# Kernel tuning notes

Hardware: AMD Instinct MI355X
Metric: run time of the kernel (lower is better)

The kernel has to match this reference:

```python
import jax, jax.numpy as jnp
import numpy as np

N = 10000        # nodes
E = 160000       # edges (avg degree 16)
MUL = 128        # channel multiplicity
A = 10           # node-attr (species one-hot) dim
RAD = 8          # radial bessel features
INV_SQRT3 = 0.5773502691896258  # CG coefficient for 1o x 1o -> 0e


def _mlp(x, Ws):
    # RadialMLP: linear layers with SiLU between, no activation on last
    for W in Ws[:-1]:
        x = jax.nn.silu(x @ W)
    return x @ Ws[-1]


def setup_inputs() -> dict:
    key = jax.random.key(0)
    ks = jax.random.split(key, 25)

    def g(k, shape):
        return jax.random.normal(k, shape, jnp.float32) / np.float32(np.sqrt(shape[0]))

    return {
        "node_attrs": jax.random.uniform(ks[0], (N, A), jnp.float32),
        "node_feats": jax.random.normal(ks[1], (N, 4 * MUL), jnp.float32),
        "edge_attrs": jax.random.normal(ks[2], (E, 4), jnp.float32),
        "edge_feats": jax.random.uniform(ks[3], (E, RAD), jnp.float32),
        "W_src": g(ks[5], (A, MUL)),
        "W_tgt": g(ks[6], (A, MUL)),
        "W_up0": g(ks[7], (MUL, MUL)),
        "W_up1": g(ks[8], (MUL, MUL)),
        "W_skip0": g(ks[9], (MUL, MUL)),
        "W_skip1": g(ks[10], (MUL, MUL)),
        "W_res0": g(ks[11], (MUL, 2 * MUL)),
        "W_res1": g(ks[12], (MUL, MUL)),
        "W_lin1_0": g(ks[13], (2 * MUL, 2 * MUL)),
        "W_lin1_1": g(ks[14], (2 * MUL, MUL)),
        "W_lin2_0": g(ks[15], (MUL, MUL)),
        "W_lin2_1": g(ks[16], (MUL, MUL)),
        "W_rad1": g(ks[17], (RAD + 2 * MUL, 64)),
        "W_rad2": g(ks[18], (64, 64)),
        "W_rad3": g(ks[19], (64, 64)),
        "W_rad4": g(ks[20], (64, 4 * MUL)),
        "W_den1": g(ks[21], (RAD + 2 * MUL, 64)),
        "W_den2": g(ks[22], (64, 1)),
        "alpha": jnp.ones((), jnp.float32),   # scaled by 20 inside (alpha = param * 20)
        "beta": jnp.zeros((), jnp.float32),
        "edge_index": jax.random.randint(ks[4], (E, 2), 0, N),
    }


def _forward(node_attrs, node_feats, edge_attrs, edge_feats,
             W_src, W_tgt, W_up0, W_up1, W_skip0, W_skip1, W_res0, W_res1,
             W_lin1_0, W_lin1_1, W_lin2_0, W_lin2_1,
             W_rad1, W_rad2, W_rad3, W_rad4, W_den1, W_den2,
             alpha, beta, edge_index):
    n = node_feats.shape[0]
    # split node feats into 128x0e scalars and 128x1o vectors (mul_ir layout)
    s = node_feats[:, :MUL]                           # [N, 128]
    v = node_feats[:, MUL:].reshape(n, MUL, 3)        # [N, 128, 3]

    # skip connection: Linear(node_feats_irreps -> hidden_irreps)
    sc_s = s @ W_skip0
    sc_v = jnp.einsum("nui,uv->nvi", v, W_skip1)
    sc = jnp.concatenate([sc_s, sc_v.reshape(n, -1)], axis=-1)  # [N, 512]

    # linear_up (node_feats -> edge_irreps) and linear_res (-> irreps_nonlin)
    up_s = s @ W_up0
    up_v = jnp.einsum("nui,uv->nvi", v, W_up1)
    res_s = s @ W_res0                                # [N, 256] (scalars + gates)
    res_v = jnp.einsum("nui,uv->nvi", v, W_res1)      # [N, 128, 3]

    # per-species scalar embeddings, gathered per edge
    src_emb = node_attrs @ W_src                      # [N, 128]
    tgt_emb = node_attrs @ W_tgt
    snd = edge_index[:, 0]
    rcv = edge_index[:, 1]
    aug = jnp.concatenate([edge_feats, src_emb[snd], tgt_emb[rcv]], axis=-1)  # [E, 264]

    # radial MLP -> per-edge tensor-product weights; density MLP
    tpw = _mlp(aug, [W_rad1, W_rad2, W_rad3, W_rad4])  # [E, 512]
    edge_density = jnp.tanh(_mlp(aug, [W_den1, W_den2]) ** 2)  # [E, 1]
    density = jax.ops.segment_sum(edge_density, rcv, num_segments=n)  # [N, 1]

    # equivariant tensor product (uvu, per-edge weights), lmax=1 CG paths
    xs = up_s[snd]                                    # [E, 128]
    xv = up_v[snd]                                    # [E, 128, 3]
    y0 = edge_attrs[:, :1]                            # [E, 1]
    y1 = edge_attrs[:, 1:4]                           # [E, 3]
    wA, wB, wC, wD = jnp.split(tpw, 4, axis=-1)
    mA = wA * xs * y0                                               # 0e x 0e -> 0e
    mD = wD * jnp.einsum("eui,ei->eu", xv, y1) * INV_SQRT3          # 1o x 1o -> 0e
    mB = (wB * xs)[:, :, None] * y1[:, None, :]                     # 0e x 1o -> 1o
    mC = wC[:, :, None] * xv * y0[:, :, None]                       # 1o x 0e -> 1o
    m_s = jnp.concatenate([mA, mD], axis=-1)          # [E, 256]
    m_v = jnp.concatenate([mB, mC], axis=1)           # [E, 256, 3]

    # scatter-add messages to receiver nodes
    msg_s = jax.ops.segment_sum(m_s, rcv, num_segments=n)  # [N, 256]
    msg_v = jax.ops.segment_sum(m_v, rcv, num_segments=n)  # [N, 256, 3]

    # linear_1 (irreps_mid -> irreps_nonlin), density normalization, residual
    msg_s = msg_s @ W_lin1_0                          # [N, 256]
    msg_v = jnp.einsum("nui,uv->nvi", msg_v, W_lin1_1)  # [N, 128, 3]
    denom = density * beta + alpha * 20.0             # [N, 1]
    msg_s = msg_s / denom + res_s
    msg_v = msg_v / denom[..., None] + res_v

    # equivariant gate nonlinearity: silu on scalars, sigmoid gates on vectors
    scal = jax.nn.silu(msg_s[:, :MUL])
    gate = jax.nn.sigmoid(msg_s[:, MUL:])
    vec = msg_v * gate[:, :, None]

    # linear_2 and reshape to [N, channels, (lmax+1)^2]
    out_s = scal @ W_lin2_0                           # [N, 128]
    out_v = jnp.einsum("nui,uv->nvi", vec, W_lin2_1)  # [N, 128, 3]
    message = jnp.concatenate([out_s[:, :, None], out_v], axis=-1)  # [N, 128, 4]
    return message, sc


def reference(node_attrs, node_feats, edge_attrs, edge_feats,
              W_src, W_tgt, W_up0, W_up1, W_skip0, W_skip1, W_res0, W_res1,
              W_lin1_0, W_lin1_1, W_lin2_0, W_lin2_1,
              W_rad1, W_rad2, W_rad3, W_rad4, W_den1, W_den2,
              alpha, beta, edge_index):
    return _forward(node_attrs, node_feats, edge_attrs, edge_feats,
                    W_src, W_tgt, W_up0, W_up1, W_skip0, W_skip1, W_res0, W_res1,
                    W_lin1_0, W_lin1_1, W_lin2_0, W_lin2_1,
                    W_rad1, W_rad2, W_rad3, W_rad4, W_den1, W_den2,
                    alpha, beta, edge_index)
```

## Files before the change

kernel.cpp:

```cpp
#include <hip/hip_runtime.h>
#include <math.h>

#define NN 10000
#define NE 160000
#define MUL 128
#define ADIM 10
#define RADF 8
#define HID 64
#define INV_SQRT3 0.57735026918962576f
#define NB64 157

typedef __attribute__((ext_vector_type(8))) short bf16x8;
typedef __attribute__((ext_vector_type(4))) float f32x4;

__device__ __forceinline__ float silu_f(float x){ return x / (1.0f + __expf(-x)); }
__device__ __forceinline__ float sigmoid_f(float x){ return 1.0f / (1.0f + __expf(-x)); }
__device__ __forceinline__ unsigned short f2b(float f){
  union{float f; unsigned u;} v; v.f=f;
  unsigned r = (v.u + 0x7fffu + ((v.u>>16)&1u))>>16;
  return (unsigned short)r;
}
__device__ __forceinline__ float b2f(unsigned short h){
  union{unsigned u; float f;} v; v.u = ((unsigned)h)<<16; return v.f;
}
__device__ __forceinline__ float b2f_lo(unsigned u){
  union{unsigned u; float f;} v; v.u = u<<16; return v.f;
}
__device__ __forceinline__ float b2f_hi(unsigned u){
  union{unsigned u; float f;} v; v.u = u & 0xffff0000u; return v.f;
}

__global__ __launch_bounds__(256) void k_nodeemb(
    const float* __restrict__ attrs, const float* __restrict__ Wc,
    float* __restrict__ pA, float* __restrict__ pB){
  int idx = blockIdx.x*256 + threadIdx.x;
  if (idx >= NN*64) return;
  int n = idx>>6, c = idx&63;
  float s0=0,s1=0,s2=0,s3=0;
  #pragma unroll
  for (int a=0;a<ADIM;a++){
    float x = attrs[n*ADIM+a];
    s0 += x*Wc[(0*ADIM+a)*64+c];
    s1 += x*Wc[(1*ADIM+a)*64+c];
    s2 += x*Wc[(2*ADIM+a)*64+c];
    s3 += x*Wc[(3*ADIM+a)*64+c];
  }
  pA[(size_t)n*128 + c*2 + 0] = s0;
  pA[(size_t)n*128 + c*2 + 1] = s2;
  pB[(size_t)n*128 + c*2 + 0] = s1;
  pB[(size_t)n*128 + c*2 + 1] = s3;
}

__global__ __launch_bounds__(256) void k_feat_prep(
    const float* __restrict__ feats, unsigned short* __restrict__ fs16,
    unsigned short* __restrict__ fv16){
  int idx = blockIdx.x*256 + threadIdx.x;
  int n = idx >> 9, c = idx & 511;
  float v = feats[idx];
  if (c < 128) fs16[n*128 + c] = f2b(v);
  else {
    int q = c - 128; int u = q/3; int i = q - 3*u;
    fv16[((size_t)n*3 + i)*128 + u] = f2b(v);
  }
}

__global__ __launch_bounds__(256) void k_prep(
    const float* __restrict__ Wr2, const float* __restrict__ Wr3,
    const float* __restrict__ Wr4,
    const float* __restrict__ Wl10, const float* __restrict__ Wl11,
    const float* __restrict__ Wl20, const float* __restrict__ Wl21,
    const float* __restrict__ Wsk0, const float* __restrict__ Wup0, const float* __restrict__ Wres0,
    const float* __restrict__ Wsk1, const float* __restrict__ Wup1, const float* __restrict__ Wres1,
    const float* __restrict__ Wsrc, const float* __restrict__ Wtgt,
    const float* __restrict__ Wr1, const float* __restrict__ Wd1,
    unsigned short* __restrict__ WTr2, unsigned short* __restrict__ WTr3,
    unsigned short* __restrict__ WTr4,
    unsigned short* __restrict__ Wl10T, unsigned short* __restrict__ Wl11T,
    unsigned short* __restrict__ Wl20T, unsigned short* __restrict__ Wl21T,
    unsigned short* __restrict__ WnsT, unsigned short* __restrict__ WnvT,
    float* __restrict__ Wc){
  int idx = blockIdx.x*256 + threadIdx.x;
  if (idx < 4096){
    int j = idx; int n=j>>6, k=j&63;
    WTr2[j] = f2b(Wr2[k*64+n]);
  } else if (idx < 8192){
    int j = idx-4096; int n=j>>6, k=j&63;
    WTr3[j] = f2b(Wr3[k*64+n]);
  } else if (idx < 40960){
    int j = idx-8192; int n=j>>6, k=j&63;
    WTr4[j] = f2b(Wr4[k*512+n]);
  } else if (idx < 106496){
    int j = idx-40960; int n=j>>8, k=j&255;
    Wl10T[j] = f2b(Wl10[k*256+n]);
  } else if (idx < 139264){
    int j = idx-106496; int n=j>>8, k=j&255;
    Wl11T[j] = f2b(Wl11[k*128+n]);
  } else if (idx < 155648){
    int j = idx-139264; int n=j>>7, k=j&127;
    Wl20T[j] = f2b(Wl20[k*128+n]);
  } else if (idx < 172032){
    int j = idx-155648; int n=j>>7, k=j&127;
    Wl21T[j] = f2b(Wl21[k*128+n]);
  } else if (idx < 237568){
    int j = idx-172032; int n=j>>7, k=j&127;
    float v;
    if (n < 128)      v = Wsk0[k*128+n];
    else if (n < 256) v = Wup0[k*128+(n-128)];
    else              v = Wres0[k*256+(n-256)];
    WnsT[j] = f2b(v);
  } else if (idx < 286720){
    int j = idx-237568; int n=j>>7, k=j&127;
    float v;
    if (n < 128)      v = Wsk1[k*128+n];
    else if (n < 256) v = Wup1[k*128+(n-128)];
    else              v = Wres1[k*128+(n-256)];
    WnvT[j] = f2b(v);
  } else if (idx < 286976){
    int j = idx - 286720;
    int m = j>>6, c = j&63;
    const float* WA = (m&1)? Wtgt : Wsrc;
    const float* WB = (m<2)? Wr1 : Wd1;
    int koff = (m&1)? 136 : 8;
    for (int a=0;a<ADIM;a++){
      float s=0.f;
      for (int k=0;k<128;k++) s += WA[a*128+k]*WB[(koff+k)*64+c];
      Wc[(m*ADIM+a)*64+c] = s;
    }
  }
}

__global__ __launch_bounds__(256) void k_node_pre2(
    const unsigned short* __restrict__ fs16, const unsigned short* __restrict__ fv16,
    const unsigned short* __restrict__ WnsT, const unsigned short* __restrict__ WnvT,
    float* __restrict__ out_sc,
    unsigned short* __restrict__ upk16,
    float* __restrict__ res_s, float* __restrict__ res_v){
  __shared__ unsigned short fA[64][136];
  int nb = blockIdx.x*64;
  int c = blockIdx.y;
  int g, ntc;
  if (c < 4){ g=0; ntc=c; } else { g = 1 + (c-4)/3; ntc = (c-4)%3; }
  int tid = threadIdx.x;
  int w = tid>>6, l = tid&63, m0 = w*16, lr = l&15, lg = l>>4;
  for (int idx=tid; idx<64*16; idx+=256){
    int row = idx>>4, s8 = idx&15;
    int n = min(nb+row, NN-1);
    const unsigned short* src = (g==0) ? &fs16[(size_t)n*128 + s8*8]
                                       : &fv16[((size_t)n*3 + (g-1))*128 + s8*8];
    *(uint4*)&fA[row][s8*8] = *(const uint4*)src;
  }
  __syncthreads();
  const unsigned short* WT = ((g==0)? WnsT : WnvT) + (size_t)ntc*128*128;
  f32x4 acc[8];
  #pragma unroll
  for (int t=0;t<8;t++) acc[t]=(f32x4)(0.f);
  #pragma unroll
  for (int kb=0;kb<4;kb++){
    bf16x8 a = *(const bf16x8*)&fA[m0+lr][kb*32 + lg*8];
    #pragma unroll
    for (int t=0;t<8;t++){
      bf16x8 b = *(const bf16x8*)&WT[(size_t)(t*16+lr)*128 + kb*32 + lg*8];
      acc[t] = __builtin_amdgcn_mfma_f32_16x16x32_bf16(a, b, acc[t], 0,0,0);
    }
  }
  #pragma unroll
  for (int t=0;t<8;t++){
    #pragma unroll
    for (int r=0;r<4;r++){
      int col = (ntc*8+t)*16 + lr;
      int row = m0 + lg*4 + r;
      int n = nb + row;
      if (n < NN){
        float v = acc[t][r];
        if (g==0){
          if (col < 128)      out_sc[(size_t)n*512 + col] = v;
          else if (col < 256){
            int cc = col-128;
            upk16[(size_t)n*512 + (cc&63)*8 + (cc>>6)] = f2b(v);
          } else              res_s[(size_t)n*256 + col-256] = v;
        } else {
          int i = g-1;
          if (col < 128)      out_sc[(size_t)n*512 + 128 + col*3 + i] = v;
          else if (col < 256){
            int cc = col-128;
            upk16[(size_t)n*512 + (cc&63)*8 + (1+i)*2 + (cc>>6)] = f2b(v);
          } else              res_v[((size_t)n*3+i)*128 + col-256] = v;
        }
      }
    }
  }
}

__global__ __launch_bounds__(256) void k_deg(const int* __restrict__ eidx, int* __restrict__ deg){
  int i = blockIdx.x*256+threadIdx.x;
  if (i<NE) atomicAdd(&deg[eidx[2*i+1]],1);
}
__global__ __launch_bounds__(256) void k_scan(const int* __restrict__ deg, int* __restrict__ offsets){
  __shared__ int part[256];
  int t = threadIdx.x; int base = t*40;
  int s=0;
  for (int k=0;k<40;k++){ int idx=base+k; if (idx<NN) s+=deg[idx]; }
  part[t]=s; __syncthreads();
  if (t==0){ int run=0; for (int i=0;i<256;i++){ int v=part[i]; part[i]=run; run+=v; } }
  __syncthreads();
  int run = part[t];
  for (int k=0;k<40;k++){
    int idx=base+k;
    if (idx<=NN) offsets[idx]=run;
    if (idx<NN) run+=deg[idx];
  }
}
__global__ __launch_bounds__(256) void k_fill(const int* __restrict__ eidx, const int* __restrict__ offsets,
                                              int* __restrict__ cursor, int* __restrict__ elist){
  int i = blockIdx.x*256+threadIdx.x;
  if (i<NE){ int r = eidx[2*i+1]; int p = atomicAdd(&cursor[r],1); elist[offsets[r]+p]=i; }
}

__global__ __launch_bounds__(256) void k_tpw(
    const int* __restrict__ elist, const int* __restrict__ eidx,
    const float* __restrict__ ef, const float* __restrict__ ea,
    const float* __restrict__ pA, const float* __restrict__ pB,
    const float* __restrict__ Wr1, const float* __restrict__ Wd1, const float* __restrict__ Wd2,
    const unsigned short* __restrict__ WTr2, const unsigned short* __restrict__ WTr3,
    const unsigned short* __restrict__ WTr4,
    const int* __restrict__ offsets, int nstart, int nend, int cap,
    unsigned* __restrict__ tpwp, float4* __restrict__ ybuf,
    int* __restrict__ sndbuf, float* __restrict__ densbuf){
  __shared__ unsigned short hA[64][72];
  __shared__ unsigned short hB[64][72];
  __shared__ float efs[64][8];
  __shared__ int s_snd[64], s_rcv[64];
  int ebase = offsets[nstart];
  int eend  = min(offsets[nend], ebase + cap);
  int i0 = ebase + blockIdx.x*64;
  if (i0 >= eend) return;
  int nrows = min(64, eend - i0);
  int tid = threadIdx.x;
  int w = tid>>6, l = tid&63, m0 = w*16, lr = l&15, lg = l>>4;
  if (tid < 64){
    int ii = min(i0 + tid, eend-1);
    int e = elist[ii];
    int sn = eidx[2*e], rc = eidx[2*e+1];
    s_snd[tid]=sn; s_rcv[tid]=rc;
    if (tid < nrows){
      int li = i0 - ebase + tid;
      sndbuf[li] = sn;
      ybuf[li] = ((const float4*)ea)[e];
    }
  }
  if (tid < 128){
    int r = tid>>1, hf = tid&1;
    int e = elist[min(i0+r, eend-1)];
    *(float4*)&efs[r][hf*4] = *(const float4*)&ef[(size_t)e*8 + hf*4];
  }
  __syncthreads();
  {
    float wr[8], wd[8];
    #pragma unroll
    for (int k=0;k<8;k++){ wr[k]=Wr1[k*64+l]; wd[k]=Wd1[k*64+l]; }
    float wd2c = Wd2[l];
    #pragma unroll
    for (int j=0;j<16;j++){
      int r = m0+j;
      int sn = s_snd[r], rc = s_rcv[r];
      float2 av = *(const float2*)&pA[(size_t)sn*128 + l*2];
      float2 bv = *(const float2*)&pB[(size_t)rc*128 + l*2];
      float h  = av.x + bv.x;
      float hd = av.y + bv.y;
      #pragma unroll
      for (int k=0;k<8;k++){ float ek=efs[r][k]; h += ek*wr[k]; hd += ek*wd[k]; }
      hA[r][l] = f2b(silu_f(h));
      float sv = silu_f(hd)*wd2c;
      #pragma unroll
      for (int m=32;m;m>>=1) sv += __shfl_xor(sv, m);
      if (l==0 && r < nrows) densbuf[i0 - ebase + r] = tanhf(sv*sv);
    }
  }
  f32x4 acc[4];
  #pragma unroll
  for (int nt=0;nt<4;nt++) acc[nt]=(f32x4)(0.f);
  #pragma unroll
  for (int kb=0;kb<2;kb++){
    bf16x8 a = *(const bf16x8*)&hA[m0+lr][kb*32 + lg*8];
    #pragma unroll
    for (int nt=0;nt<4;nt++){
      bf16x8 b = *(const bf16x8*)&WTr2[(nt*16+lr)*64 + kb*32 + lg*8];
      acc[nt] = __builtin_amdgcn_mfma_f32_16x16x32_bf16(a, b, acc[nt], 0,0,0);
    }
  }
  #pragma unroll
  for (int nt=0;nt<4;nt++)
    #pragma unroll
    for (int r=0;r<4;r++)
      hB[m0+lg*4+r][nt*16+lr] = f2b(silu_f(acc[nt][r]));
  #pragma unroll
  for (int nt=0;nt<4;nt++) acc[nt]=(f32x4)(0.f);
  #pragma unroll
  for (int kb=0;kb<2;kb++){
    bf16x8 a = *(const bf16x8*)&hB[m0+lr][kb*32 + lg*8];
    #pragma unroll
    for (int nt=0;nt<4;nt++){
      bf16x8 b = *(const bf16x8*)&WTr3[(nt*16+lr)*64 + kb*32 + lg*8];
      acc[nt] = __builtin_amdgcn_mfma_f32_16x16x32_bf16(a, b, acc[nt], 0,0,0);
    }
  }
  #pragma unroll
  for (int nt=0;nt<4;nt++)
    #pragma unroll
    for (int r=0;r<4;r++)
      hA[m0+lg*4+r][nt*16+lr] = f2b(silu_f(acc[nt][r]));
  int erow0 = i0 - ebase;
  #pragma unroll
  for (int nt=0; nt<4; nt++){
    unsigned pvv[4][4];
    #pragma unroll
    for (int G=0; G<4; G++){
      f32x4 aE=(f32x4)(0.f), aO=(f32x4)(0.f);
      #pragma unroll
      for (int kb=0; kb<2; kb++){
        bf16x8 a  = *(const bf16x8*)&hA[m0+lr][kb*32 + lg*8];
        bf16x8 bE = *(const bf16x8*)&WTr4[((2*G)*64+nt*16+lr)*64 + kb*32 + lg*8];
        bf16x8 bO = *(const bf16x8*)&WTr4[((2*G+1)*64+nt*16+lr)*64 + kb*32 + lg*8];
        aE = __builtin_amdgcn_mfma_f32_16x16x32_bf16(a, bE, aE, 0,0,0);
        aO = __builtin_amdgcn_mfma_f32_16x16x32_bf16(a, bO, aO, 0,0,0);
      }
      #pragma unroll
      for (int r=0;r<4;r++)
        pvv[r][G] = (unsigned)f2b(aE[r]) | ((unsigned)f2b(aO[r])<<16);
    }
    #pragma unroll
    for (int r=0;r<4;r++){
      int row = m0 + lg*4 + r;
      if (row < nrows)
        *(uint4*)&tpwp[(size_t)(erow0+row)*256 + (nt*16+lr)*4] = *(uint4*)&pvv[r][0];
    }
  }
}

__global__ __launch_bounds__(256) void k_gather(
    const unsigned* __restrict__ tpwp, const float4* __restrict__ ybuf,
    const int* __restrict__ sndbuf, const float* __restrict__ densbuf,
    const uint4* __restrict__ upk4,
    const int* __restrict__ offsets, int nstart,
    unsigned short* __restrict__ msg_s16, unsigned short* __restrict__ msg_v16,
    float* __restrict__ density){
  int w = threadIdx.x>>6, l = threadIdx.x&63;
  int n = nstart + blockIdx.x*4 + w;
  if (n >= NN) return;
  int ebase = offsets[nstart];
  int s0 = offsets[n], s1 = offsets[n+1];
  float mA0=0,mA1=0,mD0=0,mD1=0;
  float mB00=0,mB01=0,mB10=0,mB11=0,mB20=0,mB21=0;
  float mC00=0,mC01=0,mC10=0,mC11=0,mC20=0,mC21=0;
  float dsum=0;
  #pragma unroll 2
  for (int i=s0;i<s1;++i){
    int li = i - ebase;
    int sn = sndbuf[li];
    float4 y = ybuf[li];
    dsum += densbuf[li];
    uint4 tq = *(const uint4*)&tpwp[(size_t)li*256 + l*4];
    uint4 uq = upk4[(size_t)sn*64 + l];
    float wA0=b2f_lo(tq.x), wA1=b2f_hi(tq.x);
    float wB0=b2f_lo(tq.y), wB1=b2f_hi(tq.y);
    float wC0=b2f_lo(tq.z), wC1=b2f_hi(tq.z);
    float wD0=b2f_lo(tq.w), wD1=b2f_hi(tq.w);
    float xs0=b2f_lo(uq.x), xs1=b2f_hi(uq.x);
    float xv00=b2f_lo(uq.y), xv01=b2f_hi(uq.y);
    float xv10=b2f_lo(uq.z), xv11=b2f_hi(uq.z);
    float xv20=b2f_lo(uq.w), xv21=b2f_hi(uq.w);
    mA0 += wA0*xs0*y.x; mA1 += wA1*xs1*y.x;
    float dot0 = xv00*y.y + xv10*y.z + xv20*y.w;
    float dot1 = xv01*y.y + xv11*y.z + xv21*y.w;
    mD0 += wD0*dot0; mD1 += wD1*dot1;
    float b0 = wB0*xs0, b1 = wB1*xs1;
    mB00 += b0*y.y; mB01 += b1*y.y;
    mB10 += b0*y.z; mB11 += b1*y.z;
    mB20 += b0*y.w; mB21 += b1*y.w;
    float c0 = wC0*y.x, c1 = wC1*y.x;
    mC00 += c0*xv00; mC01 += c1*xv01;
    mC10 += c0*xv10; mC11 += c1*xv11;
    mC20 += c0*xv20; mC21 += c1*xv21;
  }
  unsigned short* ms = msg_s16 + (size_t)n*256;
  ms[l]=f2b(mA0); ms[64+l]=f2b(mA1);
  ms[128+l]=f2b(mD0*INV_SQRT3); ms[192+l]=f2b(mD1*INV_SQRT3);
  unsigned short* mv = msg_v16 + (size_t)n*768;
  mv[l]=f2b(mB00);     mv[64+l]=f2b(mB01);  mv[128+l]=f2b(mC00); mv[192+l]=f2b(mC01);
  mv[256+l]=f2b(mB10); mv[320+l]=f2b(mB11); mv[384+l]=f2b(mC10); mv[448+l]=f2b(mC11);
  mv[512+l]=f2b(mB20); mv[576+l]=f2b(mB21); mv[640+l]=f2b(mC20); mv[704+l]=f2b(mC21);
  if (l==0) density[n]=dsum;
}

__global__ __launch_bounds__(256) void k_post1(
    const unsigned short* __restrict__ msg_s16, const unsigned short* __restrict__ msg_v16,
    const float* __restrict__ density,
    const float* __restrict__ res_s, const float* __restrict__ res_v,
    const unsigned short* __restrict__ Wl10T, const unsigned short* __restrict__ Wl11T,
    const float* __restrict__ alphap, const float* __restrict__ betap,
    unsigned short* __restrict__ scal16, unsigned short* __restrict__ gate16,
    unsigned short* __restrict__ vtmp16){
  __shared__ unsigned short sm[64][264];
  __shared__ float sden[64];
  int nb = blockIdx.x*64, y = blockIdx.y;
  int tid = threadIdx.x;
  int w = tid>>6, l = tid&63, m0 = w*16, lr = l&15, lg = l>>4;
  for (int idx=tid; idx<64*32; idx+=256){
    int row = idx>>5, s8 = idx&31;
    int n = min(nb+row, NN-1);
    const unsigned short* src = (y<2)? &msg_s16[(size_t)n*256 + s8*8]
                                     : &msg_v16[(size_t)n*768 + (y-2)*256 + s8*8];
    *(uint4*)&sm[row][s8*8] = *(const uint4*)src;
  }
  if (tid < 64){
    int n = min(nb+tid, NN-1);
    sden[tid] = density[n]*betap[0] + alphap[0]*20.0f;
  }
  __syncthreads();
  const unsigned short* BT = (y<2)? (Wl10T + (size_t)y*128*256) : Wl11T;
  f32x4 acc[8];
  #pragma unroll
  for (int t=0;t<8;t++) acc[t]=(f32x4)(0.f);
  for (int kb=0;kb<8;kb++){
    bf16x8 a = *(const bf16x8*)&sm[m0+lr][kb*32 + lg*8];
    #pragma unroll
    for (int t=0;t<8;t++){
      bf16x8 b = *(const bf16x8*)&BT[(size_t)(t*16+lr)*256 + kb*32 + lg*8];
      acc[t] = __builtin_amdgcn_mfma_f32_16x16x32_bf16(a, b, acc[t], 0,0,0);
    }
  }
  #pragma unroll
  for (int t=0;t<8;t++){
    #pragma unroll
    for (int r=0;r<4;r++){
      int col = t*16+lr;
      int row = m0 + lg*4 + r;
      int n = nb + row;
      if (n < NN){
        float v = acc[t][r]/sden[row];
        if (y==0){
          v += res_s[(size_t)n*256 + col];
          scal16[(size_t)n*128 + col] = f2b(silu_f(v));
        } else if (y==1){
          v += res_s[(size_t)n*256 + 128 + col];
          gate16[(size_t)n*128 + col] = f2b(sigmoid_f(v));
        } else {
          int i = y-2;
          v += res_v[((size_t)n*3+i)*128 + col];
          vtmp16[((size_t)i*NN + n)*128 + col] = f2b(v);
        }
      }
    }
  }
}

__global__ __launch_bounds__(256) void k_post2(
    const unsigned short* __restrict__ scal16, const unsigned short* __restrict__ gate16,
    const unsigned short* __restrict__ vtmp16,
    const unsigned short* __restrict__ Wl20T, const unsigned short* __restrict__ Wl21T,
    float* __restrict__ out_msg){
  __shared__ unsigned short sA[64][136];
  int nb = blockIdx.x*64, y = blockIdx.y;
  int tid = threadIdx.x;
  int w = tid>>6, l = tid&63, m0 = w*16, lr = l&15, lg = l>>4;
  for (int idx=tid; idx<64*16; idx+=256){
    int row = idx>>4, s8 = idx&15;
    int n = min(nb+row, NN-1);
    if (y==0){
      *(uint4*)&sA[row][s8*8] = *(const uint4*)&scal16[(size_t)n*128 + s8*8];
    } else {
      int i = y-1;
      uint4 va = *(const uint4*)&vtmp16[((size_t)i*NN + n)*128 + s8*8];
      uint4 vg = *(const uint4*)&gate16[(size_t)n*128 + s8*8];
      const unsigned short* pa = (const unsigned short*)&va;
      const unsigned short* pg = (const unsigned short*)&vg;
      unsigned short o[8];
      #pragma unroll
      for (int j=0;j<8;j++) o[j] = f2b(b2f(pa[j])*b2f(pg[j]));
      *(uint4*)&sA[row][s8*8] = *(const uint4*)o;
    }
  }
  __syncthreads();
  const unsigned short* BT = (y==0)? Wl20T : Wl21T;
  f32x4 acc[8];
  #pragma unroll
  for (int t=0;t<8;t++) acc[t]=(f32x4)(0.f);
  #pragma unroll
  for (int kb=0;kb<4;kb++){
    bf16x8 a = *(const bf16x8*)&sA[m0+lr][kb*32 + lg*8];
    #pragma unroll
    for (int t=0;t<8;t++){
      bf16x8 b = *(const bf16x8*)&BT[(size_t)(t*16+lr)*128 + kb*32 + lg*8];
      acc[t] = __builtin_amdgcn_mfma_f32_16x16x32_bf16(a, b, acc[t], 0,0,0);
    }
  }
  #pragma unroll
  for (int t=0;t<8;t++){
    #pragma unroll
    for (int r=0;r<4;r++){
      int col = t*16+lr;
      int n = nb + m0 + lg*4 + r;
      if (n < NN) out_msg[(size_t)n*512 + col*4 + y] = acc[t][r];
    }
  }
}

extern "C" void kernel_launch(void* const* d_in, const int* in_sizes, int n_in,
                              void* d_out, int out_size, void* d_ws, size_t ws_size,
                              hipStream_t stream){
  (void)in_sizes; (void)n_in; (void)out_size;
  const float* attrs = (const float*)d_in[0];
  const float* feats = (const float*)d_in[1];
  const float* ea    = (const float*)d_in[2];
  const float* ef    = (const float*)d_in[3];
  const float* Wsrc  = (const float*)d_in[4];
  const float* Wtgt  = (const float*)d_in[5];
  const float* Wup0  = (const float*)d_in[6];
  const float* Wup1  = (const float*)d_in[7];
  const float* Wsk0  = (const float*)d_in[8];
  const float* Wsk1  = (const float*)d_in[9];
  const float* Wres0 = (const float*)d_in[10];
  const float* Wres1 = (const float*)d_in[11];
  const float* Wl10  = (const float*)d_in[12];
  const float* Wl11  = (const float*)d_in[13];
  const float* Wl20  = (const float*)d_in[14];
  const float* Wl21  = (const float*)d_in[15];
  const float* Wr1   = (const float*)d_in[16];
  const float* Wr2   = (const float*)d_in[17];
  const float* Wr3   = (const float*)d_in[18];
  const float* Wr4   = (const float*)d_in[19];
  const float* Wd1   = (const float*)d_in[20];
  const float* Wd2   = (const float*)d_in[21];
  const float* alphap= (const float*)d_in[22];
  const float* betap = (const float*)d_in[23];
  const int*   eidx  = (const int*)d_in[24];

  const size_t fixed_bytes =
      (size_t)NN*(512 + 1536 + 1024 + 1536 + 4 + 1024 + 256 + 768 + 512 + 512 + 256) +
      (size_t)286976*2 + 4*ADIM*64*4 +
      (10240+10240+10256)*4 + (size_t)NE*4 + 64*256;
  int nchunk, npc, cap;
  if (fixed_bytes + (size_t)NE*1048 + 65536 <= ws_size){ nchunk=1; npc=NN;   cap=NE;    }
  else if (fixed_bytes + 81920ULL*1048 + 65536 <= ws_size){ nchunk=2; npc=5000; cap=81920; }
  else { nchunk=4; npc=2500; cap=44032; }

  char* p = (char*)d_ws;
  auto alloc = [&](size_t bytes)->char*{ char* r=p; p += (bytes+255)&~(size_t)255; return r; };
  unsigned* tpwp  = (unsigned*)alloc((size_t)cap*256*4);
  unsigned short* msg_s16 = (unsigned short*)alloc((size_t)NN*256*2);
  unsigned short* msg_v16 = (unsigned short*)alloc((size_t)NN*768*2);
  float*  res_s   = (float*)alloc((size_t)NN*256*4);
  float*  res_v   = (float*)alloc((size_t)NN*384*4);
  float*  density = (float*)alloc((size_t)NN*4);
  float4* ybuf    = (float4*)alloc((size_t)cap*16);
  float*  densbuf = (float*)alloc((size_t)cap*4);
  int*    sndbuf  = (int*)alloc((size_t)cap*4);
  uint4*  upk     = (uint4*)alloc((size_t)NN*64*16);
  unsigned short* fs16 = (unsigned short*)alloc((size_t)NN*128*2);
  unsigned short* fv16 = (unsigned short*)alloc((size_t)NN*384*2);
  float* pA = (float*)alloc((size_t)NN*128*4);
  float* pB = (float*)alloc((size_t)NN*128*4);
  float* Wc  = (float*)alloc(4*ADIM*64*4);
  unsigned short* gate16 = (unsigned short*)alloc((size_t)NN*128*2);
  unsigned short* WTr2 = (unsigned short*)alloc(4096*2);
  unsigned short* WTr3 = (unsigned short*)alloc(4096*2);
  unsigned short* WTr4 = (unsigned short*)alloc(32768*2);
  unsigned short* Wl10T = (unsigned short*)alloc(65536*2);
  unsigned short* Wl11T = (unsigned short*)alloc(32768*2);
  unsigned short* Wl20T = (unsigned short*)alloc(16384*2);
  unsigned short* Wl21T = (unsigned short*)alloc(16384*2);
  unsigned short* WnsT  = (unsigned short*)alloc(65536*2);
  unsigned short* WnvT  = (unsigned short*)alloc(49152*2);
  int* deg     = (int*)alloc(10240*4);
  int* cursor  = (int*)alloc(10240*4);
  int* offsets = (int*)alloc(10256*4);
  int* elist   = (int*)alloc((size_t)NE*4);

  unsigned short* scal16 = fs16;
  unsigned short* vtmp16 = fv16;

  float* out_msg = (float*)d_out;
  float* out_sc  = out_msg + (size_t)NN*512;

  hipMemsetAsync(deg, 0, 2*10240*sizeof(int), stream);

  k_prep<<<1121, 256, 0, stream>>>(Wr2, Wr3, Wr4, Wl10, Wl11, Wl20, Wl21,
                                   Wsk0, Wup0, Wres0, Wsk1, Wup1, Wres1,
                                   Wsrc, Wtgt, Wr1, Wd1,
                                   WTr2, WTr3, WTr4,
                                   Wl10T, Wl11T, Wl20T, Wl21T, WnsT, WnvT, Wc);
  k_nodeemb<<<(NN*64+255)/256, 256, 0, stream>>>(attrs, Wc, pA, pB);
  k_feat_prep<<<NN*512/256, 256, 0, stream>>>(feats, fs16, fv16);
  k_node_pre2<<<dim3(NB64,13), 256, 0, stream>>>(fs16, fv16, WnsT, WnvT,
                                                 out_sc, (unsigned short*)upk, res_s, res_v);
  k_deg<<<(NE+255)/256, 256, 0, stream>>>(eidx, deg);
  k_scan<<<1, 256, 0, stream>>>(deg, offsets);
  k_fill<<<(NE+255)/256, 256, 0, stream>>>(eidx, offsets, cursor, elist);

  int tpw_blocks = (cap+63)/64;
  for (int c=0; c<nchunk; ++c){
    k_tpw<<<tpw_blocks, 256, 0, stream>>>(elist, eidx, ef, ea, pA, pB,
                                          Wr1, Wd1, Wd2, WTr2, WTr3, WTr4,
                                          offsets, c*npc, (c+1)*npc, cap,
                                          tpwp, ybuf, sndbuf, densbuf);
    k_gather<<<npc/4, 256, 0, stream>>>(tpwp, ybuf, sndbuf, densbuf, upk,
                                        offsets, c*npc, msg_s16, msg_v16, density);
  }

  k_post1<<<dim3(NB64,5), 256, 0, stream>>>(msg_s16, msg_v16, density, res_s, res_v,
                                            Wl10T, Wl11T, alphap, betap,
                                            scal16, gate16, vtmp16);
  k_post2<<<dim3(NB64,4), 256, 0, stream>>>(scal16, gate16, vtmp16,
                                            Wl20T, Wl21T, out_msg);
}
```

Baseline: 446.2 us.

## Split gather edge loop across two waves per node and use HIP bf16 conversions

The gather kernel now assigns two wavefronts to each destination node, each handling alternate edges. The partial sums are combined through shared memory before the bf16 stores. The aim is more memory-level parallelism for the irregular per-node edge traversal, at the cost of a block-wide sync and some LDS traffic. Manual float-to-bf16 rounding is also replaced by the HIP intrinsics, including a packed two-value conversion, which may map to hardware convert instructions. The per-node early-exit bound check was removed, which relies on npc dividing evenly.

```diff
diff --git a/kernel.cpp b/kernel.cpp
--- a/kernel.cpp
+++ b/kernel.cpp
@@ -1,4 +1,5 @@
 #include <hip/hip_runtime.h>
+#include <hip/hip_bf16.h>
 #include <math.h>
 
 #define NN 10000
@@ -20,6 +21,15 @@
   unsigned r = (v.u + 0x7fffu + ((v.u>>16)&1u))>>16;
   return (unsigned short)r;
 }
+__device__ __forceinline__ unsigned short f2bh(float f){
+  __hip_bfloat16 h = __float2bfloat16(f);
+  union{ __hip_bfloat16 h; unsigned short u; } v; v.h=h; return v.u;
+}
+__device__ __forceinline__ unsigned f2b2(float lo, float hi){
+  float2 t; t.x=lo; t.y=hi;
+  __hip_bfloat162 h2 = __float22bfloat162_rn(t);
+  union{ __hip_bfloat162 h; unsigned u; } v; v.h=h2; return v.u;
+}
 __device__ __forceinline__ float b2f(unsigned short h){
   union{unsigned u; float f;} v; v.u = ((unsigned)h)<<16; return v.f;
 }
@@ -57,10 +67,10 @@
   int idx = blockIdx.x*256 + threadIdx.x;
   int n = idx >> 9, c = idx & 511;
   float v = feats[idx];
-  if (c < 128) fs16[n*128 + c] = f2b(v);
+  if (c < 128) fs16[n*128 + c] = f2bh(v);
   else {
     int q = c - 128; int u = q/3; int i = q - 3*u;
-    fv16[((size_t)n*3 + i)*128 + u] = f2b(v);
+    fv16[((size_t)n*3 + i)*128 + u] = f2bh(v);
   }
 }
 
@@ -176,14 +186,14 @@
           if (col < 128)      out_sc[(size_t)n*512 + col] = v;
           else if (col < 256){
             int cc = col-128;
-            upk16[(size_t)n*512 + (cc&63)*8 + (cc>>6)] = f2b(v);
+            upk16[(size_t)n*512 + (cc&63)*8 + (cc>>6)] = f2bh(v);
           } else              res_s[(size_t)n*256 + col-256] = v;
         } else {
           int i = g-1;
           if (col < 128)      out_sc[(size_t)n*512 + 128 + col*3 + i] = v;
           else if (col < 256){
             int cc = col-128;
-            upk16[(size_t)n*512 + (cc&63)*8 + (1+i)*2 + (cc>>6)] = f2b(v);
+            upk16[(size_t)n*512 + (cc&63)*8 + (1+i)*2 + (cc>>6)] = f2bh(v);
           } else              res_v[((size_t)n*3+i)*128 + col-256] = v;
         }
       }
@@ -269,7 +279,7 @@
       float hd = av.y + bv.y;
       #pragma unroll
       for (int k=0;k<8;k++){ float ek=efs[r][k]; h += ek*wr[k]; hd += ek*wd[k]; }
-      hA[r][l] = f2b(silu_f(h));
+      hA[r][l] = f2bh(silu_f(h));
       float sv = silu_f(hd)*wd2c;
       #pragma unroll
       for (int m=32;m;m>>=1) sv += __shfl_xor(sv, m);
@@ -292,7 +302,7 @@
   for (int nt=0;nt<4;nt++)
     #pragma unroll
     for (int r=0;r<4;r++)
-      hB[m0+lg*4+r][nt*16+lr] = f2b(silu_f(acc[nt][r]));
+      hB[m0+lg*4+r][nt*16+lr] = f2bh(silu_f(acc[nt][r]));
   #pragma unroll
   for (int nt=0;nt<4;nt++) acc[nt]=(f32x4)(0.f);
   #pragma unroll
@@ -308,7 +318,7 @@
   for (int nt=0;nt<4;nt++)
     #pragma unroll
     for (int r=0;r<4;r++)
-      hA[m0+lg*4+r][nt*16+lr] = f2b(silu_f(acc[nt][r]));
+      hA[m0+lg*4+r][nt*16+lr] = f2bh(silu_f(acc[nt][r]));
   int erow0 = i0 - ebase;
   #pragma unroll
   for (int nt=0; nt<4; nt++){
@@ -326,7 +336,7 @@
       }
       #pragma unroll
       for (int r=0;r<4;r++)
-        pvv[r][G] = (unsigned)f2b(aE[r]) | ((unsigned)f2b(aO[r])<<16);
+        pvv[r][G] = f2b2(aE[r], aO[r]);
     }
     #pragma unroll
     for (int r=0;r<4;r++){
@@ -344,17 +354,18 @@
     const int* __restrict__ offsets, int nstart,
     unsigned short* __restrict__ msg_s16, unsigned short* __restrict__ msg_v16,
     float* __restrict__ density){
+  __shared__ float part[2][1024];
+  __shared__ float pden[2];
   int w = threadIdx.x>>6, l = threadIdx.x&63;
-  int n = nstart + blockIdx.x*4 + w;
-  if (n >= NN) return;
+  int pairIdx = w>>1, half = w&1;
+  int n = nstart + blockIdx.x*2 + pairIdx;
   int ebase = offsets[nstart];
   int s0 = offsets[n], s1 = offsets[n+1];
   float mA0=0,mA1=0,mD0=0,mD1=0;
   float mB00=0,mB01=0,mB10=0,mB11=0,mB20=0,mB21=0;
   float mC00=0,mC01=0,mC10=0,mC11=0,mC20=0,mC21=0;
   float dsum=0;
-  #pragma unroll 2
-  for (int i=s0;i<s1;++i){
+  for (int i=s0+half; i<s1; i+=2){
     int li = i - ebase;
     int sn = sndbuf[li];
     float4 y = ybuf[li];
@@ -382,14 +393,31 @@
     mC10 += c0*xv10; mC11 += c1*xv11;
     mC20 += c0*xv20; mC21 += c1*xv21;
   }
-  unsigned short* ms = msg_s16 + (size_t)n*256;
-  ms[l]=f2b(mA0); ms[64+l]=f2b(mA1);
-  ms[128+l]=f2b(mD0*INV_SQRT3); ms[192+l]=f2b(mD1*INV_SQRT3);
-  unsigned short* mv = msg_v16 + (size_t)n*768;
-  mv[l]=f2b(mB00);     mv[64+l]=f2b(mB01);  mv[128+l]=f2b(mC00); mv[192+l]=f2b(mC01);
-  mv[256+l]=f2b(mB10); mv[320+l]=f2b(mB11); mv[384+l]=f2b(mC10); mv[448+l]=f2b(mC11);
-  mv[512+l]=f2b(mB20); mv[576+l]=f2b(mB21); mv[640+l]=f2b(mC20); mv[704+l]=f2b(mC21);
-  if (l==0) density[n]=dsum;
+  if (half==1){
+    float* P = part[pairIdx];
+    P[0*64+l]=mA0;  P[1*64+l]=mA1;  P[2*64+l]=mD0;  P[3*64+l]=mD1;
+    P[4*64+l]=mB00; P[5*64+l]=mB01; P[6*64+l]=mB10; P[7*64+l]=mB11;
+    P[8*64+l]=mB20; P[9*64+l]=mB21; P[10*64+l]=mC00; P[11*64+l]=mC01;
+    P[12*64+l]=mC10; P[13*64+l]=mC11; P[14*64+l]=mC20; P[15*64+l]=mC21;
+    if (l==0) pden[pairIdx]=dsum;
+  }
+  __syncthreads();
+  if (half==0){
+    const float* P = part[pairIdx];
+    mA0+=P[0*64+l];  mA1+=P[1*64+l];  mD0+=P[2*64+l];  mD1+=P[3*64+l];
+    mB00+=P[4*64+l]; mB01+=P[5*64+l]; mB10+=P[6*64+l]; mB11+=P[7*64+l];
+    mB20+=P[8*64+l]; mB21+=P[9*64+l]; mC00+=P[10*64+l]; mC01+=P[11*64+l];
+    mC10+=P[12*64+l]; mC11+=P[13*64+l]; mC20+=P[14*64+l]; mC21+=P[15*64+l];
+    dsum += pden[pairIdx];
+    unsigned short* ms = msg_s16 + (size_t)n*256;
+    ms[l]=f2bh(mA0); ms[64+l]=f2bh(mA1);
+    ms[128+l]=f2bh(mD0*INV_SQRT3); ms[192+l]=f2bh(mD1*INV_SQRT3);
+    unsigned short* mv = msg_v16 + (size_t)n*768;
+    mv[l]=f2bh(mB00);     mv[64+l]=f2bh(mB01);  mv[128+l]=f2bh(mC00); mv[192+l]=f2bh(mC01);
+    mv[256+l]=f2bh(mB10); mv[320+l]=f2bh(mB11); mv[384+l]=f2bh(mC10); mv[448+l]=f2bh(mC11);
+    mv[512+l]=f2bh(mB20); mv[576+l]=f2bh(mB21); mv[640+l]=f2bh(mC20); mv[704+l]=f2bh(mC21);
+    if (l==0) density[n]=dsum;
+  }
 }
 
 __global__ __launch_bounds__(256) void k_post1(
@@ -440,14 +468,14 @@
         float v = acc[t][r]/sden[row];
         if (y==0){
           v += res_s[(size_t)n*256 + col];
-          scal16[(size_t)n*128 + col] = f2b(silu_f(v));
+          scal16[(size_t)n*128 + col] = f2bh(silu_f(v));
         } else if (y==1){
           v += res_s[(size_t)n*256 + 128 + col];
-          gate16[(size_t)n*128 + col] = f2b(sigmoid_f(v));
+          gate16[(size_t)n*128 + col] = f2bh(sigmoid_f(v));
         } else {
           int i = y-2;
           v += res_v[((size_t)n*3+i)*128 + col];
-          vtmp16[((size_t)i*NN + n)*128 + col] = f2b(v);
+          vtmp16[((size_t)i*NN + n)*128 + col] = f2bh(v);
         }
       }
     }
@@ -476,7 +504,7 @@
       const unsigned short* pg = (const unsigned short*)&vg;
       unsigned short o[8];
       #pragma unroll
-      for (int j=0;j<8;j++) o[j] = f2b(b2f(pa[j])*b2f(pg[j]));
+      for (int j=0;j<8;j++) o[j] = f2bh(b2f(pa[j])*b2f(pg[j]));
       *(uint4*)&sA[row][s8*8] = *(const uint4*)o;
     }
   }
@@ -603,7 +631,7 @@
                                           Wr1, Wd1, Wd2, WTr2, WTr3, WTr4,
                                           offsets, c*npc, (c+1)*npc, cap,
                                           tpwp, ybuf, sndbuf, densbuf);
-    k_gather<<<npc/4, 256, 0, stream>>>(tpwp, ybuf, sndbuf, densbuf, upk,
+    k_gather<<<npc/2, 256, 0, stream>>>(tpwp, ybuf, sndbuf, densbuf, upk,
                                         offsets, c*npc, msg_s16, msg_v16, density);
   }
 
```

Result: no change. 440.5 us (-1.3%).
